# Kernel optimization log

Hardware: AMD Instinct MI355X
Metric: run time of the kernel (lower is better)

## Reference

```python
import jax, jax.numpy as jnp
import numpy as np
import math

N, D, C = 1024, 512, 70722
M_MARGIN = 0.4
H_SCALE = 0.333
S_SCALE = 64.0
EPS = 0.001


def setup_inputs() -> dict:
    key = jax.random.key(0)
    k1, k2, k3 = jax.random.split(key, 3)
    x = jax.random.normal(k1, (N, D), dtype=jnp.float32)
    labels = jax.random.randint(k2, (N,), 0, C, dtype=jnp.int64)
    # weights ~ N(0, 0.01) as in nn.Parameter init
    weights = 0.01 * jax.random.normal(k3, (C, D), dtype=jnp.float32)
    return {"x": x, "labels": labels, "weights": weights}


def reference(x, labels, weights):
    # world_size == 1: all-gather is identity and all labels are local.
    x_norms = jnp.maximum(jnp.linalg.norm(x, axis=1, keepdims=True), 1e-8)  # [N,1]

    norm_emb = x / jnp.maximum(jnp.linalg.norm(x, axis=1, keepdims=True), 1e-12)
    norm_w = weights / jnp.maximum(jnp.linalg.norm(weights, axis=1, keepdims=True), 1e-12)
    cosine = jnp.clip(norm_emb @ norm_w.T, -1.0, 1.0)  # [N,C]

    # AdaFace adaptive margin scaler (detached norms; t_alpha=1 -> batch stats = current stats)
    safe_norms = jax.lax.stop_gradient(jnp.clip(x_norms, 0.001, 100.0))  # [N,1]
    batch_mean = jnp.mean(safe_norms)
    batch_std = jnp.std(safe_norms, ddof=1)  # torch .std() is unbiased
    margin_scaler = jnp.clip((safe_norms - batch_mean) / (batch_std + EPS) * H_SCALE, -1.0, 1.0)  # [N,1]

    g_angular = -M_MARGIN * margin_scaler           # [N,1]
    g_add = M_MARGIN + M_MARGIN * margin_scaler     # [N,1]

    onehot = jax.nn.one_hot(labels, C, dtype=cosine.dtype)  # [N,C]

    theta = jnp.arccos(cosine)
    theta_m = jnp.clip(theta + onehot * g_angular, EPS, math.pi - EPS)
    logits = (jnp.cos(theta_m) - onehot * g_add) * S_SCALE  # [N,C]

    logp = jax.nn.log_softmax(logits, axis=-1)
    loss = -jnp.mean(jnp.take_along_axis(logp, labels[:, None], axis=1))
    return loss
```

## Files before the change

kernel.cpp:

```cpp
#include <hip/hip_runtime.h>
#include <hip/hip_bf16.h>
#include <stdint.h>

#define DIM 512
#define NROWS 1024
#define NCLS 70722

typedef float floatx4 __attribute__((ext_vector_type(4)));

__device__ __forceinline__ unsigned pk4_fp8(float a, float b, float c, float d) {
    unsigned v = 0;
    v = __builtin_amdgcn_cvt_pk_fp8_f32(a, b, v, false);
    v = __builtin_amdgcn_cvt_pk_fp8_f32(c, d, v, true);
    return v;
}

__device__ __forceinline__ float wave_reduce_sum(float s) {
    #pragma unroll
    for (int m = 1; m < 64; m <<= 1) s += __shfl_xor(s, m);
    return s;
}

__global__ __launch_bounds__(256) void prep_kernel(
        const float* __restrict__ x, const float* __restrict__ W,
        const int* __restrict__ labels,
        uint8_t* __restrict__ An, uint8_t* __restrict__ Wn8,
        float* __restrict__ rownorm, float* __restrict__ coslab,
        float* __restrict__ rowsum) {
    int b = blockIdx.x;
    int wv = threadIdx.x >> 6, lane = threadIdx.x & 63;
    if (b < NROWS / 4) {
        if (threadIdx.x < 4) rowsum[b * 4 + threadIdx.x] = 0.0f;
        int row = b * 4 + wv;
        int lab = labels[row];
        const float4* xs = (const float4*)(x + (size_t)row * DIM);
        const float4* ws = (const float4*)(W + (size_t)lab * DIM);
        float4 xa = xs[lane * 2], xb = xs[lane * 2 + 1];
        float4 wa = ws[lane * 2], wb = ws[lane * 2 + 1];
        float dxx = xa.x*xa.x + xa.y*xa.y + xa.z*xa.z + xa.w*xa.w
                  + xb.x*xb.x + xb.y*xb.y + xb.z*xb.z + xb.w*xb.w;
        float dww = wa.x*wa.x + wa.y*wa.y + wa.z*wa.z + wa.w*wa.w
                  + wb.x*wb.x + wb.y*wb.y + wb.z*wb.z + wb.w*wb.w;
        float dxw = xa.x*wa.x + xa.y*wa.y + xa.z*wa.z + xa.w*wa.w
                  + xb.x*wb.x + xb.y*wb.y + xb.z*wb.z + xb.w*wb.w;
        dxx = wave_reduce_sum(dxx);
        dww = wave_reduce_sum(dww);
        dxw = wave_reduce_sum(dxw);
        float norm = sqrtf(dxx);
        float s16 = 16.0f / fmaxf(norm, 1e-12f);
        uint2 p;
        p.x = pk4_fp8(xa.x*s16, xa.y*s16, xa.z*s16, xa.w*s16);
        p.y = pk4_fp8(xb.x*s16, xb.y*s16, xb.z*s16, xb.w*s16);
        *(uint2*)(An + (size_t)row * DIM + lane * 8) = p;
        if (lane == 0) {
            rownorm[row] = norm;
            coslab[row]  = dxw / (fmaxf(norm, 1e-12f) * fmaxf(sqrtf(dww), 1e-12f));
        }
    } else {
        int c = (b - NROWS / 4) * 4 + wv;
        if (c < NCLS) {
            const float4* src = (const float4*)(W + (size_t)c * DIM);
            float4 va = src[lane * 2], vb = src[lane * 2 + 1];
            float ss = va.x*va.x + va.y*va.y + va.z*va.z + va.w*va.w
                     + vb.x*vb.x + vb.y*vb.y + vb.z*vb.z + vb.w*vb.w;
            ss = wave_reduce_sum(ss);
            float s16 = 16.0f / fmaxf(sqrtf(ss), 1e-12f);
            uint2 p;
            p.x = pk4_fp8(va.x*s16, va.y*s16, va.z*s16, va.w*s16);
            p.y = pk4_fp8(vb.x*s16, vb.y*s16, vb.z*s16, vb.w*s16);
            *(uint2*)(Wn8 + (size_t)c * DIM + lane * 8) = p;
        }
    }
}

__global__ __launch_bounds__(512, 2) void gemm7_kernel(
        const uint8_t* __restrict__ An, const uint8_t* __restrict__ Wn8,
        float* __restrict__ rowsum) {
    __shared__ uint8_t Asm[128 * 512];
    __shared__ uint8_t Bsm[2][256 * 128];
    __shared__ float red[128];

    int b = blockIdx.x;
    int mgrp = b >> 5, cgrp = b & 31;
    int tid = threadIdx.x, lane = tid & 63, wv = tid >> 6;
    if (tid < 128) red[tid] = 0.0f;

    int arow = tid >> 5;
    int aq = ((tid & 31) ^ (arow & 7)) * 16;
    const uint8_t* aGb = An + (size_t)(mgrp * 128 + arow) * DIM + aq;

    int brow = lane >> 3;
    int ckB = ((lane & 7) ^ brow) * 16;

    int wm = (wv >> 2) * 64, wn = (wv & 3) * 64;
    int fr = lane & 15, fq = lane >> 4;
    int fh = fq >> 1, fl = (fq & 1) * 8;

    const floatx4 vzero = {0.0f, 0.0f, 0.0f, 0.0f};
    floatx4 acc[4][4] = {};
    float srun[4][4] = {};
    long af[4][16];

#define GLL(gp, lp) __builtin_amdgcn_global_load_lds( \
        (const __attribute__((address_space(1))) unsigned int*)(gp), \
        (__attribute__((address_space(3))) unsigned int*)(lp), 16, 0, 0)
#define BAR  __builtin_amdgcn_s_barrier()
#define FEN  asm volatile("" ::: "memory")

    #pragma unroll
    for (int i = 0; i < 8; ++i)
        GLL(aGb + i * 8192, Asm + i * 8192 + wv * 1024);

    const uint8_t *bp0, *bp1, *bp2, *bp3;
    {
        int cb = cgrp * 256 + wv * 32 + brow;
        bp0 = Wn8 + (size_t)min(cb,      NCLS - 1) * DIM + ckB;
        bp1 = Wn8 + (size_t)min(cb + 8,  NCLS - 1) * DIM + ckB;
        bp2 = Wn8 + (size_t)min(cb + 16, NCLS - 1) * DIM + ckB;
        bp3 = Wn8 + (size_t)min(cb + 24, NCLS - 1) * DIM + ckB;
    }

#define STAGE_B(slot, kb) do { \
        uint8_t* _d = Bsm[slot] + wv * 4096; \
        GLL(bp0 + (kb), _d); \
        GLL(bp1 + (kb), _d + 1024); \
        GLL(bp2 + (kb), _d + 2048); \
        GLL(bp3 + (kb), _d + 3072); } while (0)

    STAGE_B(0, 0);
    asm volatile("s_waitcnt vmcnt(4)" ::: "memory");
    BAR;

    #pragma unroll
    for (int m = 0; m < 4; ++m) {
        int R = wm + m * 16 + fr;
        const uint8_t* rp = Asm + R * 512 + fl;
        #pragma unroll
        for (int ksl = 0; ksl < 16; ++ksl)
            af[m][ksl] = *(const long*)(rp + (((2 * ksl + fh) ^ (R & 7)) * 16));
    }

#define COMPUTE(slot, KSB) do { \
        _Pragma("unroll") \
        for (int n = 0; n < 4; ++n) { \
            int R = wn + n * 16 + fr; \
            const uint8_t* rp = Bsm[slot] + R * 128 + fl; \
            long bg[4]; \
            _Pragma("unroll") \
            for (int ks = 0; ks < 4; ++ks) \
                bg[ks] = *(const long*)(rp + (((ks * 2 + fh) ^ (R & 7)) * 16)); \
            _Pragma("unroll") \
            for (int ks = 0; ks < 4; ++ks) \
                _Pragma("unroll") \
                for (int m = 0; m < 4; ++m) \
                    acc[m][n] = __builtin_amdgcn_mfma_f32_16x16x32_fp8_fp8( \
                        af[m][(KSB) + ks], bg[ks], acc[m][n], 0, 0, 0); \
        } \
    } while (0)

    int nct = (cgrp < 21) ? 9 : 8;
    int c = cgrp;
    for (int ct = 0; ct < nct; ++ct) {
        STAGE_B(1, 128);
        asm volatile("s_waitcnt vmcnt(4)" ::: "memory");
        BAR;
        __builtin_amdgcn_s_setprio(1); COMPUTE(0, 0);  __builtin_amdgcn_s_setprio(0);
        FEN; BAR;
        STAGE_B(0, 256);
        asm volatile("s_waitcnt vmcnt(4)" ::: "memory");
        BAR;
        __builtin_amdgcn_s_setprio(1); COMPUTE(1, 4);  __builtin_amdgcn_s_setprio(0);
        FEN; BAR;
        STAGE_B(1, 384);
        asm volatile("s_waitcnt vmcnt(4)" ::: "memory");
        BAR;
        __builtin_amdgcn_s_setprio(1); COMPUTE(0, 8);  __builtin_amdgcn_s_setprio(0);
        FEN; BAR;
        if (ct != nct - 1) {
            int cb = (c + 32) * 256 + wv * 32 + brow;
            bp0 = Wn8 + (size_t)min(cb,      NCLS - 1) * DIM + ckB;
            bp1 = Wn8 + (size_t)min(cb + 8,  NCLS - 1) * DIM + ckB;
            bp2 = Wn8 + (size_t)min(cb + 16, NCLS - 1) * DIM + ckB;
            bp3 = Wn8 + (size_t)min(cb + 24, NCLS - 1) * DIM + ckB;
            STAGE_B(0, 0);
            asm volatile("s_waitcnt vmcnt(4)" ::: "memory");
        } else {
            asm volatile("s_waitcnt vmcnt(0)" ::: "memory");
        }
        BAR;
        __builtin_amdgcn_s_setprio(1); COMPUTE(1, 12); __builtin_amdgcn_s_setprio(0);
        FEN; BAR;

        {
            const float CLIPC = 0.99999950f;
            const float ISCL  = 1.0f / 256.0f;
            int colbase = c * 256 + wn + fr;
            #pragma unroll
            for (int m = 0; m < 4; ++m) {
                #pragma unroll
                for (int reg = 0; reg < 4; ++reg) {
                    float s = 0.0f;
                    #pragma unroll
                    for (int n = 0; n < 4; ++n) {
                        int col = colbase + n * 16;
                        float cc = acc[m][n][reg] * ISCL;
                        cc = fminf(fmaxf(cc, -CLIPC), CLIPC);
                        float term = __expf(64.0f * cc - 64.0f);
                        s += (col < NCLS) ? term : 0.0f;
                    }
                    srun[m][reg] += s;
                }
            }
            #pragma unroll
            for (int m = 0; m < 4; ++m)
                #pragma unroll
                for (int n = 0; n < 4; ++n)
                    acc[m][n] = vzero;
        }
        c += 32;
    }

#undef GLL
#undef STAGE_B
#undef COMPUTE
#undef BAR
#undef FEN

    #pragma unroll
    for (int m = 0; m < 4; ++m) {
        #pragma unroll
        for (int reg = 0; reg < 4; ++reg) {
            float s = srun[m][reg];
            s += __shfl_xor(s, 1); s += __shfl_xor(s, 2);
            s += __shfl_xor(s, 4); s += __shfl_xor(s, 8);
            if (fr == 0) atomicAdd(&red[wm + m * 16 + fq * 4 + reg], s);
        }
    }
    __syncthreads();
    if (tid < 128) atomicAdd(rowsum + mgrp * 128 + tid, red[tid]);
}

__global__ __launch_bounds__(1024) void finalize_kernel(
        const float* __restrict__ rowsum, const float* __restrict__ coslab,
        const float* __restrict__ rownorm, float* __restrict__ out) {
    __shared__ float part[16];
    __shared__ float bc[2];
    int t = threadIdx.x, lane = t & 63, w = t >> 6;
    float v = fminf(fmaxf(rownorm[t], 0.001f), 100.0f);

    float s = wave_reduce_sum(v);
    if (lane == 0) part[w] = s;
    __syncthreads();
    if (t < 64) {
        float p = (lane < 16) ? part[lane] : 0.0f;
        p = wave_reduce_sum(p);
        if (lane == 0) bc[0] = p * (1.0f / 1024.0f);
    }
    __syncthreads();
    float mean = bc[0];
    float d = v - mean;

    s = wave_reduce_sum(d * d);
    if (lane == 0) part[w] = s;
    __syncthreads();
    if (t < 64) {
        float p = (lane < 16) ? part[lane] : 0.0f;
        p = wave_reduce_sum(p);
        if (lane == 0) bc[1] = sqrtf(p * (1.0f / 1023.0f));
    }
    __syncthreads();
    float stdv = bc[1];

    float ms = d / (stdv + 0.001f) * 0.333f;
    ms = fminf(fmaxf(ms, -1.0f), 1.0f);
    float g_ang = -0.4f * ms;
    float g_add =  0.4f + 0.4f * ms;
    const float CLIPC = 0.99999950f;
    const float PI = 3.14159265358979323846f;
    float cl  = fminf(fmaxf(coslab[t], -1.0f), 1.0f);
    float cne = fminf(fmaxf(cl, -CLIPC), CLIPC);
    float logit_non = 64.0f * cne;
    float theta = acosf(cl);
    float tm = fminf(fmaxf(theta + g_ang, 0.001f), PI - 0.001f);
    float logit_true = (__cosf(tm) - g_add) * 64.0f;
    float ssum = rowsum[t] - __expf(logit_non - 64.0f) + __expf(logit_true - 64.0f);
    float loss = logf(ssum) + 64.0f - logit_true;

    s = wave_reduce_sum(loss);
    if (lane == 0) part[w] = s;
    __syncthreads();
    if (t < 64) {
        float p = (lane < 16) ? part[lane] : 0.0f;
        p = wave_reduce_sum(p);
        if (lane == 0) out[0] = p * (1.0f / 1024.0f);
    }
}

extern "C" void kernel_launch(void* const* d_in, const int* in_sizes, int n_in,
                              void* d_out, int out_size, void* d_ws, size_t ws_size,
                              hipStream_t stream) {
    const float* x      = (const float*)d_in[0];
    const int*   labels = (const int*)d_in[1];
    const float* W      = (const float*)d_in[2];
    float* out = (float*)d_out;
    char* ws = (char*)d_ws;

    const size_t SZ_WN8 = 36212736;
    const size_t SZ_AN  = 524288;
    uint8_t* Wn8 = (uint8_t*)ws;
    uint8_t* An  = (uint8_t*)(ws + SZ_WN8);
    float* rownorm = (float*)(ws + SZ_WN8 + SZ_AN);
    float* rowsum  = rownorm + 1024;
    float* coslab  = rowsum + 1024;

    int wblocks = (NCLS + 3) / 4;
    prep_kernel<<<NROWS / 4 + wblocks, 256, 0, stream>>>(
        x, W, labels, An, Wn8, rownorm, coslab, rowsum);
    gemm7_kernel<<<256, 512, 0, stream>>>(An, Wn8, rowsum);
    finalize_kernel<<<1, 1024, 0, stream>>>(rowsum, coslab, rownorm, out);
}
```

Baseline: 292.1 us.

## Pre-tile fp8 operands into MFMA fragment layout and load B directly from global

The prep kernel now writes the normalized fp8 activations and weights in a 16-row tiled layout that matches the MFMA 16x16x32 fragment order, with each wave packing 16 weight rows. The GEMM kernel drops the LDS staging, double buffering and barriers, and loads A and B fragments straight from global memory as 8-byte vector loads. The per-row partial sums are reduced into LDS after every column tile instead of being held in registers. This removes LDS traffic and barrier overhead, but it gives up the explicit prefetch pipeline, so global latency now depends on the compiler and on occupancy. Many more LDS atomics are issued.

```diff
diff --git a/kernel.cpp b/kernel.cpp
--- a/kernel.cpp
+++ b/kernel.cpp
@@ -5,6 +5,7 @@
 #define DIM 512
 #define NROWS 1024
 #define NCLS 70722
+#define NC16 4421
 
 typedef float floatx4 __attribute__((ext_vector_type(4)));
 
@@ -24,7 +25,7 @@
 __global__ __launch_bounds__(256) void prep_kernel(
         const float* __restrict__ x, const float* __restrict__ W,
         const int* __restrict__ labels,
-        uint8_t* __restrict__ An, uint8_t* __restrict__ Wn8,
+        uint8_t* __restrict__ AnT, uint8_t* __restrict__ WT,
         float* __restrict__ rownorm, float* __restrict__ coslab,
         float* __restrict__ rowsum) {
     int b = blockIdx.x;
@@ -51,145 +52,95 @@
         uint2 p;
         p.x = pk4_fp8(xa.x*s16, xa.y*s16, xa.z*s16, xa.w*s16);
         p.y = pk4_fp8(xb.x*s16, xb.y*s16, xb.z*s16, xb.w*s16);
-        *(uint2*)(An + (size_t)row * DIM + lane * 8) = p;
+        *(uint2*)(AnT + (size_t)(row >> 4) * 8192 + lane * 128 + (row & 15) * 8) = p;
         if (lane == 0) {
             rownorm[row] = norm;
             coslab[row]  = dxw / (fmaxf(norm, 1e-12f) * fmaxf(sqrtf(dww), 1e-12f));
         }
     } else {
-        int c = (b - NROWS / 4) * 4 + wv;
-        if (c < NCLS) {
-            const float4* src = (const float4*)(W + (size_t)c * DIM);
-            float4 va = src[lane * 2], vb = src[lane * 2 + 1];
-            float ss = va.x*va.x + va.y*va.y + va.z*va.z + va.w*va.w
-                     + vb.x*vb.x + vb.y*vb.y + vb.z*vb.z + vb.w*vb.w;
-            ss = wave_reduce_sum(ss);
-            float s16 = 16.0f / fmaxf(sqrtf(ss), 1e-12f);
-            uint2 p;
-            p.x = pk4_fp8(va.x*s16, va.y*s16, va.z*s16, va.w*s16);
-            p.y = pk4_fp8(vb.x*s16, vb.y*s16, vb.z*s16, vb.w*s16);
-            *(uint2*)(Wn8 + (size_t)c * DIM + lane * 8) = p;
-        }
-    }
-}
-
-__global__ __launch_bounds__(512, 2) void gemm7_kernel(
-        const uint8_t* __restrict__ An, const uint8_t* __restrict__ Wn8,
+        int g = (b - NROWS / 4) * 4 + wv;
+        if (g < NC16) {
+            uint2 p[16];
+            #pragma unroll
+            for (int i = 0; i < 16; ++i) {
+                int c = g * 16 + i;
+                float4 va = {0.f, 0.f, 0.f, 0.f}, vb = {0.f, 0.f, 0.f, 0.f};
+                if (c < NCLS) {
+                    const float4* src = (const float4*)(W + (size_t)c * DIM);
+                    va = src[lane * 2]; vb = src[lane * 2 + 1];
+                }
+                float ss = va.x*va.x + va.y*va.y + va.z*va.z + va.w*va.w
+                         + vb.x*vb.x + vb.y*vb.y + vb.z*vb.z + vb.w*vb.w;
+                ss = wave_reduce_sum(ss);
+                float s16 = 16.0f / fmaxf(sqrtf(ss), 1e-12f);
+                p[i].x = pk4_fp8(va.x*s16, va.y*s16, va.z*s16, va.w*s16);
+                p[i].y = pk4_fp8(vb.x*s16, vb.y*s16, vb.z*s16, vb.w*s16);
+            }
+            uint8_t* dst = WT + (size_t)g * 8192 + lane * 128;
+            #pragma unroll
+            for (int j = 0; j < 8; ++j) {
+                uint4 q;
+                q.x = p[2*j].x;   q.y = p[2*j].y;
+                q.z = p[2*j+1].x; q.w = p[2*j+1].y;
+                *(uint4*)(dst + j * 16) = q;
+            }
+        }
+    }
+}
+
+__global__ __launch_bounds__(512) void gemm8_kernel(
+        const uint8_t* __restrict__ AnT, const uint8_t* __restrict__ WT,
         float* __restrict__ rowsum) {
-    __shared__ uint8_t Asm[128 * 512];
-    __shared__ uint8_t Bsm[2][256 * 128];
     __shared__ float red[128];
-
     int b = blockIdx.x;
     int mgrp = b >> 5, cgrp = b & 31;
     int tid = threadIdx.x, lane = tid & 63, wv = tid >> 6;
-    if (tid < 128) red[tid] = 0.0f;
-
-    int arow = tid >> 5;
-    int aq = ((tid & 31) ^ (arow & 7)) * 16;
-    const uint8_t* aGb = An + (size_t)(mgrp * 128 + arow) * DIM + aq;
-
-    int brow = lane >> 3;
-    int ckB = ((lane & 7) ^ brow) * 16;
 
     int wm = (wv >> 2) * 64, wn = (wv & 3) * 64;
     int fr = lane & 15, fq = lane >> 4;
-    int fh = fq >> 1, fl = (fq & 1) * 8;
+
+    long af[4][16];
+    const uint8_t* ab = AnT + (size_t)(mgrp * 8 + (wm >> 4)) * 8192 + fq * 128 + fr * 8;
+    #pragma unroll
+    for (int m = 0; m < 4; ++m)
+        #pragma unroll
+        for (int ksl = 0; ksl < 16; ++ksl)
+            af[m][ksl] = *(const long*)(ab + m * 8192 + ksl * 512);
+
+    if (tid < 128) red[tid] = 0.0f;
+    __syncthreads();
 
     const floatx4 vzero = {0.0f, 0.0f, 0.0f, 0.0f};
     floatx4 acc[4][4] = {};
-    float srun[4][4] = {};
-    long af[4][16];
-
-#define GLL(gp, lp) __builtin_amdgcn_global_load_lds( \
-        (const __attribute__((address_space(1))) unsigned int*)(gp), \
-        (__attribute__((address_space(3))) unsigned int*)(lp), 16, 0, 0)
-#define BAR  __builtin_amdgcn_s_barrier()
-#define FEN  asm volatile("" ::: "memory")
-
-    #pragma unroll
-    for (int i = 0; i < 8; ++i)
-        GLL(aGb + i * 8192, Asm + i * 8192 + wv * 1024);
-
-    const uint8_t *bp0, *bp1, *bp2, *bp3;
-    {
-        int cb = cgrp * 256 + wv * 32 + brow;
-        bp0 = Wn8 + (size_t)min(cb,      NCLS - 1) * DIM + ckB;
-        bp1 = Wn8 + (size_t)min(cb + 8,  NCLS - 1) * DIM + ckB;
-        bp2 = Wn8 + (size_t)min(cb + 16, NCLS - 1) * DIM + ckB;
-        bp3 = Wn8 + (size_t)min(cb + 24, NCLS - 1) * DIM + ckB;
-    }
-
-#define STAGE_B(slot, kb) do { \
-        uint8_t* _d = Bsm[slot] + wv * 4096; \
-        GLL(bp0 + (kb), _d); \
-        GLL(bp1 + (kb), _d + 1024); \
-        GLL(bp2 + (kb), _d + 2048); \
-        GLL(bp3 + (kb), _d + 3072); } while (0)
-
-    STAGE_B(0, 0);
-    asm volatile("s_waitcnt vmcnt(4)" ::: "memory");
-    BAR;
-
-    #pragma unroll
-    for (int m = 0; m < 4; ++m) {
-        int R = wm + m * 16 + fr;
-        const uint8_t* rp = Asm + R * 512 + fl;
-        #pragma unroll
-        for (int ksl = 0; ksl < 16; ++ksl)
-            af[m][ksl] = *(const long*)(rp + (((2 * ksl + fh) ^ (R & 7)) * 16));
-    }
-
-#define COMPUTE(slot, KSB) do { \
-        _Pragma("unroll") \
-        for (int n = 0; n < 4; ++n) { \
-            int R = wn + n * 16 + fr; \
-            const uint8_t* rp = Bsm[slot] + R * 128 + fl; \
-            long bg[4]; \
-            _Pragma("unroll") \
-            for (int ks = 0; ks < 4; ++ks) \
-                bg[ks] = *(const long*)(rp + (((ks * 2 + fh) ^ (R & 7)) * 16)); \
-            _Pragma("unroll") \
-            for (int ks = 0; ks < 4; ++ks) \
-                _Pragma("unroll") \
-                for (int m = 0; m < 4; ++m) \
-                    acc[m][n] = __builtin_amdgcn_mfma_f32_16x16x32_fp8_fp8( \
-                        af[m][(KSB) + ks], bg[ks], acc[m][n], 0, 0, 0); \
-        } \
-    } while (0)
 
     int nct = (cgrp < 21) ? 9 : 8;
     int c = cgrp;
     for (int ct = 0; ct < nct; ++ct) {
-        STAGE_B(1, 128);
-        asm volatile("s_waitcnt vmcnt(4)" ::: "memory");
-        BAR;
-        __builtin_amdgcn_s_setprio(1); COMPUTE(0, 0);  __builtin_amdgcn_s_setprio(0);
-        FEN; BAR;
-        STAGE_B(0, 256);
-        asm volatile("s_waitcnt vmcnt(4)" ::: "memory");
-        BAR;
-        __builtin_amdgcn_s_setprio(1); COMPUTE(1, 4);  __builtin_amdgcn_s_setprio(0);
-        FEN; BAR;
-        STAGE_B(1, 384);
-        asm volatile("s_waitcnt vmcnt(4)" ::: "memory");
-        BAR;
-        __builtin_amdgcn_s_setprio(1); COMPUTE(0, 8);  __builtin_amdgcn_s_setprio(0);
-        FEN; BAR;
-        if (ct != nct - 1) {
-            int cb = (c + 32) * 256 + wv * 32 + brow;
-            bp0 = Wn8 + (size_t)min(cb,      NCLS - 1) * DIM + ckB;
-            bp1 = Wn8 + (size_t)min(cb + 8,  NCLS - 1) * DIM + ckB;
-            bp2 = Wn8 + (size_t)min(cb + 16, NCLS - 1) * DIM + ckB;
-            bp3 = Wn8 + (size_t)min(cb + 24, NCLS - 1) * DIM + ckB;
-            STAGE_B(0, 0);
-            asm volatile("s_waitcnt vmcnt(4)" ::: "memory");
-        } else {
-            asm volatile("s_waitcnt vmcnt(0)" ::: "memory");
-        }
-        BAR;
-        __builtin_amdgcn_s_setprio(1); COMPUTE(1, 12); __builtin_amdgcn_s_setprio(0);
-        FEN; BAR;
+        const uint8_t* bb[4];
+        #pragma unroll
+        for (int n = 0; n < 4; ++n) {
+            int g = min(c * 16 + (wn >> 4) + n, NC16 - 1);
+            bb[n] = WT + (size_t)g * 8192 + fq * 128 + fr * 8;
+        }
+        #pragma unroll
+        for (int kb = 0; kb < 4; ++kb) {
+            long bg[4][4];
+            #pragma unroll
+            for (int n = 0; n < 4; ++n)
+                #pragma unroll
+                for (int ks = 0; ks < 4; ++ks)
+                    bg[n][ks] = *(const long*)(bb[n] + kb * 2048 + ks * 512);
+            __builtin_amdgcn_s_setprio(1);
+            #pragma unroll
+            for (int ks = 0; ks < 4; ++ks)
+                #pragma unroll
+                for (int m = 0; m < 4; ++m)
+                    #pragma unroll
+                    for (int n = 0; n < 4; ++n)
+                        acc[m][n] = __builtin_amdgcn_mfma_f32_16x16x32_fp8_fp8(
+                            af[m][kb * 4 + ks], bg[n][ks], acc[m][n], 0, 0, 0);
+            __builtin_amdgcn_s_setprio(0);
+        }
 
         {
             const float CLIPC = 0.99999950f;
@@ -208,7 +159,9 @@
                         float term = __expf(64.0f * cc - 64.0f);
                         s += (col < NCLS) ? term : 0.0f;
                     }
-                    srun[m][reg] += s;
+                    s += __shfl_xor(s, 1); s += __shfl_xor(s, 2);
+                    s += __shfl_xor(s, 4); s += __shfl_xor(s, 8);
+                    if (fr == 0) atomicAdd(&red[wm + m * 16 + fq * 4 + reg], s);
                 }
             }
             #pragma unroll
@@ -220,22 +173,6 @@
         c += 32;
     }
 
-#undef GLL
-#undef STAGE_B
-#undef COMPUTE
-#undef BAR
-#undef FEN
-
-    #pragma unroll
-    for (int m = 0; m < 4; ++m) {
-        #pragma unroll
-        for (int reg = 0; reg < 4; ++reg) {
-            float s = srun[m][reg];
-            s += __shfl_xor(s, 1); s += __shfl_xor(s, 2);
-            s += __shfl_xor(s, 4); s += __shfl_xor(s, 8);
-            if (fr == 0) atomicAdd(&red[wm + m * 16 + fq * 4 + reg], s);
-        }
-    }
     __syncthreads();
     if (tid < 128) atomicAdd(rowsum + mgrp * 128 + tid, red[tid]);
 }
@@ -305,17 +242,17 @@
     float* out = (float*)d_out;
     char* ws = (char*)d_ws;
 
-    const size_t SZ_WN8 = 36212736;
-    const size_t SZ_AN  = 524288;
-    uint8_t* Wn8 = (uint8_t*)ws;
-    uint8_t* An  = (uint8_t*)(ws + SZ_WN8);
-    float* rownorm = (float*)(ws + SZ_WN8 + SZ_AN);
+    const size_t SZ_WT = (size_t)NC16 * 8192;
+    const size_t SZ_AN = 524288;
+    uint8_t* WT  = (uint8_t*)ws;
+    uint8_t* AnT = (uint8_t*)(ws + SZ_WT);
+    float* rownorm = (float*)(ws + SZ_WT + SZ_AN);
     float* rowsum  = rownorm + 1024;
     float* coslab  = rowsum + 1024;
 
-    int wblocks = (NCLS + 3) / 4;
+    int wblocks = (NC16 + 3) / 4;
     prep_kernel<<<NROWS / 4 + wblocks, 256, 0, stream>>>(
-        x, W, labels, An, Wn8, rownorm, coslab, rowsum);
-    gemm7_kernel<<<256, 512, 0, stream>>>(An, Wn8, rowsum);
+        x, W, labels, AnT, WT, rownorm, coslab, rowsum);
+    gemm8_kernel<<<256, 512, 0, stream>>>(AnT, WT, rowsum);
     finalize_kernel<<<1, 1024, 0, stream>>>(rowsum, coslab, rownorm, out);
 }
```

New measurement: 295.8 us. No clear change (+1.3%).
